# Optimization experiments

Measured on AMD Instinct MI355X. Metric: run time of the kernel, lower is better.

Reference implementation:

```python
import jax, jax.numpy as jnp
import numpy as np

B, T, D, H = 2, 2048, 1024, 16  # batch, seq, hidden, heads; head_dim = 64


def setup_inputs() -> dict:
    key = jax.random.key(0)
    k1, k2, k3 = jax.random.split(key, 3)
    X = jax.random.normal(k1, (B, T, D), dtype=jnp.float32)
    # Dense(3*hidden_dim, use_bias=False): kernel [D, 3D]
    Wqkv = jax.random.normal(k2, (D, 3 * D), dtype=jnp.float32) / np.float32(np.sqrt(D))
    # Dense(hidden_dim, use_bias=False): kernel [D, D]
    Wproj = jax.random.normal(k3, (D, D), dtype=jnp.float32) / np.float32(np.sqrt(D))
    return {"X": X, "Wqkv": Wqkv, "Wproj": Wproj, "train": 0}


def reference(X, Wqkv, Wproj, train):
    # train=0 -> dropout is identity; the chunked online-softmax in the
    # original is mathematically exact softmax causal attention.
    b, t, d = X.shape
    hd = d // H
    qkv = X @ Wqkv                      # [B,T,3D]
    q, k, v = jnp.split(qkv, 3, axis=-1)
    q = q.reshape(b, t, H, hd)
    k = k.reshape(b, t, H, hd)
    v = v.reshape(b, t, H, hd)
    scale = 1.0 / jnp.sqrt(jnp.asarray(hd, dtype=X.dtype))
    scores = jnp.einsum('bqhd,bkhd->bhqk', q * scale, k)  # [B,H,T,T]
    causal = jnp.tril(jnp.ones((t, t), dtype=bool))
    scores = jnp.where(causal[None, None, :, :], scores, -jnp.inf)
    attn = jax.nn.softmax(scores, axis=-1)
    out = jnp.einsum('bhqk,bkhd->bqhd', attn, v).reshape(b, t, d)
    return out @ Wproj
```

## Files before the change

### kernel.cpp

```cpp
#include <hip/hip_runtime.h>


using u16 = unsigned short;
using u32 = unsigned int;

typedef __bf16 bf16x8 __attribute__((ext_vector_type(8)));
typedef __bf16 bf16x2 __attribute__((ext_vector_type(2)));
typedef float f32x4 __attribute__((ext_vector_type(4)));

#define DEV __device__ __forceinline__

DEV u16 f2bf(float f) { __bf16 h = (__bf16)f; return *(u16*)&h; }

DEV float bf2f(u16 v) {
  union { u32 u; float f; } x; x.u = (u32)v << 16; return x.f;
}

DEV u32 pk2(float lo, float hi) {
  bf16x2 t = {(__bf16)lo, (__bf16)hi};
  return *(u32*)&t;
}

DEV f32x4 mfma16(bf16x8 a, bf16x8 b, f32x4 c) {
  return __builtin_amdgcn_mfma_f32_16x16x32_bf16(a, b, c, 0, 0, 0);
}

DEV void gload_lds16(const void* g, void* l) {
  __builtin_amdgcn_global_load_lds(
      (const __attribute__((address_space(1))) void*)g,
      (__attribute__((address_space(3))) void*)l, 16, 0, 0);
}

DEV bf16x8 ld16(const u16* p) { return *(const bf16x8*)p; }

DEV void BAR() {
  __builtin_amdgcn_s_barrier();
  __builtin_amdgcn_sched_barrier(0);
}

DEV int vperm(int slot) {
  return ((((slot >> 4) & 2) | ((slot >> 2) & 1)) << 4) + (((slot >> 3) & 3) << 2) + (slot & 3);
}
DEV int vperm_inv(int k) {
  return (k & 0x23) | ((k & 0x10) >> 2) | ((k & 0x0c) << 1);
}


__global__ __launch_bounds__(256) void prep_kernel(
    const float* __restrict__ X, u16* __restrict__ Xb,
    const float* __restrict__ Wqkv, u16* __restrict__ Wqkvt,
    const float* __restrict__ Wproj, u16* __restrict__ Wprojt) {
  const int bid = blockIdx.x;
  const int t = threadIdx.x;

  if (bid < 2048) {
    int i = (bid * 256 + t) * 8;
    float4 a = *(const float4*)&X[i];
    float4 b = *(const float4*)&X[i + 4];
    union { u16 u[8]; uint4 v; } o;
    o.u[0] = f2bf(a.x); o.u[1] = f2bf(a.y); o.u[2] = f2bf(a.z); o.u[3] = f2bf(a.w);
    o.u[4] = f2bf(b.x); o.u[5] = f2bf(b.y); o.u[6] = f2bf(b.z); o.u[7] = f2bf(b.w);
    *(uint4*)&Xb[i] = o.v;
    return;
  }

  __shared__ float tile[64][65];
  const float* W; u16* Wt; int C, tb;
  if (bid < 2816) { W = Wqkv;  Wt = Wqkvt;  C = 3072; tb = bid - 2048; }
  else            { W = Wproj; Wt = Wprojt; C = 1024; tb = bid - 2816; }
  const int tilesC = C >> 6;
  const int tr = tb / tilesC, tc = tb % tilesC;
#pragma unroll
  for (int j = 0; j < 16; ++j) {
    int idx = j * 256 + t;
    int r = idx >> 6, c = idx & 63;
    tile[r][c] = W[(tr * 64 + r) * C + tc * 64 + c];
  }
  __syncthreads();
#pragma unroll
  for (int j = 0; j < 16; ++j) {
    int idx = j * 256 + t;
    int r = idx >> 6, c = idx & 63;
    Wt[(tc * 64 + r) * 1024 + tr * 64 + c] = f2bf(tile[c][r]);
  }
}


__global__ __launch_bounds__(512, 2) void gemm256_qkv_kernel(
    const u16* __restrict__ A, const u16* __restrict__ Bt,
    u16* __restrict__ Qb, u16* __restrict__ Kb, u16* __restrict__ VtP) {
  int bid = blockIdx.x;
  int bid2 = (bid & 7) * 32 + (bid >> 3);
  const int mt = bid2 >> 4, nt = bid2 & 15;
  const int m0 = mt * 256, n0 = nt * 192;
  const int tid = threadIdx.x;
  const int wid = tid >> 6, lane = tid & 63;
  const int g = lane >> 4, li = lane & 15;
  const int wm = wid >> 2, wn = wid & 3;

  __shared__ __align__(16) u16 lds[57344];

  const int srow = lane >> 3;
  const int scol = ((lane & 7) * 8) ^ ((srow & 7) << 3);

  auto ISSUE_A = [&](int s, int kt) {
    const int p = kt & 1;
#pragma unroll
    for (int is2 = 0; is2 < 2; ++is2) {
      int row = is2 * 64 + wid * 8 + srow;
      gload_lds16(&A[(size_t)(m0 + s * 128 + row) * 1024 + kt * 64 + scol],
                  &lds[s * 16384 + p * 8192 + is2 * 4096 + wid * 512]);
    }
  };
  auto ISSUE_B = [&](int kt) {
    const int p = kt & 1;
#pragma unroll
    for (int j = 0; j < 3; ++j) {
      int chunk = wid * 3 + j;
      int row = chunk * 8 + srow;
      gload_lds16(&Bt[(size_t)(n0 + row) * 1024 + kt * 64 + scol],
                  &lds[32768 + p * 12288 + chunk * 512]);
    }
  };

  auto LDA = [&](int p, int ks, bf16x8* aF) {
#pragma unroll
    for (int mi = 0; mi < 8; ++mi) {
      int row = mi * 16 + li;
      aF[mi] = ld16(&lds[wm * 16384 + p * 8192 + row * 64 +
                         ((ks * 32 + g * 8) ^ ((li & 7) << 3))]);
    }
  };
  auto LDB = [&](int p, int ks, bf16x8* bF) {
#pragma unroll
    for (int ni = 0; ni < 3; ++ni) {
      int row = wn * 48 + ni * 16 + li;
      bF[ni] = ld16(&lds[32768 + p * 12288 + row * 64 +
                         ((ks * 32 + g * 8) ^ ((li & 7) << 3))]);
    }
  };

  f32x4 acc[8][3] = {};
  bf16x8 a0[8], a1[8], bF[3];

  ISSUE_A(0, 0); ISSUE_A(1, 0); ISSUE_B(0);
  ISSUE_A(0, 1); ISSUE_A(1, 1);
  asm volatile("s_waitcnt vmcnt(4)" ::: "memory");
  BAR();

  for (int t = 0; t < 16; ++t) {
    const int p = t & 1;
    LDB(p, 0, bF);
    LDA(p, 0, a0);
    if (t + 1 < 16) ISSUE_B(t + 1);
    BAR();
    __builtin_amdgcn_s_setprio(1);
#pragma unroll
    for (int mi = 0; mi < 4; ++mi)
#pragma unroll
      for (int ni = 0; ni < 3; ++ni)
        acc[mi][ni] = mfma16(a0[mi], bF[ni], acc[mi][ni]);
    __builtin_amdgcn_s_setprio(0);
    BAR();
    LDA(p, 1, a1);
    BAR();
    __builtin_amdgcn_s_setprio(1);
#pragma unroll
    for (int mi = 4; mi < 8; ++mi)
#pragma unroll
      for (int ni = 0; ni < 3; ++ni)
        acc[mi][ni] = mfma16(a0[mi], bF[ni], acc[mi][ni]);
    __builtin_amdgcn_s_setprio(0);
    BAR();
    LDB(p, 1, bF);
    BAR();
    __builtin_amdgcn_s_setprio(1);
#pragma unroll
    for (int mi = 0; mi < 4; ++mi)
#pragma unroll
      for (int ni = 0; ni < 3; ++ni)
        acc[mi][ni] = mfma16(a1[mi], bF[ni], acc[mi][ni]);
    __builtin_amdgcn_s_setprio(0);
    BAR();
    if (t + 2 < 16) { ISSUE_A(0, t + 2); ISSUE_A(1, t + 2); }
    BAR();
    __builtin_amdgcn_s_setprio(1);
#pragma unroll
    for (int mi = 4; mi < 8; ++mi)
#pragma unroll
      for (int ni = 0; ni < 3; ++ni)
        acc[mi][ni] = mfma16(a1[mi], bF[ni], acc[mi][ni]);
    __builtin_amdgcn_s_setprio(0);
    if (t + 2 < 16) {
      asm volatile("s_waitcnt vmcnt(4)" ::: "memory");
    } else {
      asm volatile("s_waitcnt vmcnt(0)" ::: "memory");
    }
    BAR();
  }

#pragma unroll
  for (int mi = 0; mi < 8; ++mi)
#pragma unroll
    for (int ni = 0; ni < 3; ++ni) {
      int cc = n0 + wn * 48 + ni * 16 + li;
      int which = cc >> 10, rem = cc & 1023;
      int h = rem >> 6, dd = rem & 63;
      int rbase = m0 + wm * 128 + mi * 16 + g * 4;
      int bb = rbase >> 11, tt = rbase & 2047;
      if (which == 2) {
        int slot0 = (tt & ~63) + vperm_inv(tt & 63);
        size_t di = ((size_t)(bb * 16 + h) * 64 + dd) * 2048 + slot0;
        uint2 wv;
        wv.x = pk2(acc[mi][ni][0], acc[mi][ni][1]);
        wv.y = pk2(acc[mi][ni][2], acc[mi][ni][3]);
        *(uint2*)&VtP[di] = wv;
      } else {
        u16* dst = which == 0 ? Qb : Kb;
        float sc = which == 0 ? 0.18033688f : 1.0f;
        size_t di = ((size_t)(bb * 16 + h) * 2048 + tt) * 64 + dd;
#pragma unroll
        for (int r = 0; r < 4; ++r) dst[di + (size_t)r * 64] = f2bf(acc[mi][ni][r] * sc);
      }
    }
}

__global__ __launch_bounds__(256) void gemm_proj_kernel(
    const u16* __restrict__ A, const u16* __restrict__ Bt, float* __restrict__ OF) {
  constexpr int NTN = 1024 / 128;
  const int mt = blockIdx.x / NTN, nt = blockIdx.x % NTN;
  const int m0 = mt * 128, n0 = nt * 128;
  const int tid = threadIdx.x;
  const int wid = tid >> 6, lane = tid & 63;
  const int g = lane >> 4, li = lane & 15;
  const int wm = wid >> 1, wn = wid & 1;

  __shared__ __align__(16) u16 As[2][128 * 64];
  __shared__ __align__(16) u16 Bs[2][128 * 64];

  f32x4 acc[4][4] = {};

  auto ISSUE = [&](int buf, int kt) {
#pragma unroll
    for (int iss = 0; iss < 4; ++iss) {
      int e = iss * 2048 + wid * 512 + lane * 8;
      int row = e >> 6;
      int kk = (e & 63) ^ ((row & 7) << 3);
      gload_lds16(&A[(size_t)(m0 + row) * 1024 + kt * 64 + kk], &As[buf][iss * 2048 + wid * 512]);
      gload_lds16(&Bt[(size_t)(n0 + row) * 1024 + kt * 64 + kk], &Bs[buf][iss * 2048 + wid * 512]);
    }
  };

  ISSUE(0, 0);
  __syncthreads();
  int cur = 0;

  for (int kt = 0; kt < 16; ++kt) {
    if (kt + 1 < 16) ISSUE(cur ^ 1, kt + 1);
#pragma unroll
    for (int ks = 0; ks < 2; ++ks) {
      bf16x8 af[4], bfr[4];
#pragma unroll
      for (int mi = 0; mi < 4; ++mi)
        af[mi] = ld16(&As[cur][(wm * 64 + mi * 16 + li) * 64 +
                               ((ks * 32 + g * 8) ^ ((li & 7) << 3))]);
#pragma unroll
      for (int ni = 0; ni < 4; ++ni)
        bfr[ni] = ld16(&Bs[cur][(wn * 64 + ni * 16 + li) * 64 +
                                ((ks * 32 + g * 8) ^ ((li & 7) << 3))]);
#pragma unroll
      for (int mi = 0; mi < 4; ++mi)
#pragma unroll
        for (int ni = 0; ni < 4; ++ni)
          acc[mi][ni] = mfma16(af[mi], bfr[ni], acc[mi][ni]);
    }
    __syncthreads();
    cur ^= 1;
  }

#pragma unroll
  for (int mi = 0; mi < 4; ++mi)
#pragma unroll
    for (int ni = 0; ni < 4; ++ni)
#pragma unroll
      for (int r = 0; r < 4; ++r) {
        int rr = m0 + wm * 64 + mi * 16 + g * 4 + r;
        int cc = n0 + wn * 64 + ni * 16 + li;
        OF[(size_t)rr * 1024 + cc] = acc[mi][ni][r];
      }
}


__global__ __launch_bounds__(256) void attn_kernel(const u16* __restrict__ Q,
                                                   const u16* __restrict__ K,
                                                   const u16* __restrict__ VtP,
                                                   u16* __restrict__ AO,
                                                   u16* __restrict__ P2O,
                                                   float* __restrict__ L1,
                                                   float* __restrict__ L2) {
  const int bid = blockIdx.x;
  const int idx = bid >> 5;
  const int qt = 31 - (idx >> 1);
  const int half = idx & 1;
  const int bh = bid & 31;
  const int b = bh >> 4, h = bh & 15;
  const int tid = threadIdx.x;
  const int wid = tid >> 6, lane = tid & 63;
  const int g = lane >> 4, li = lane & 15;
  const int q0 = qt * 64;
  const int kmid = (qt + 2) >> 1;
  const int k0 = half ? kmid : 0;
  const int k1 = half ? qt + 1 : kmid;

  if (k0 >= k1) {
    if (tid < 64) L2[(size_t)bh * 2048 + q0 + tid] = 0.f;
    return;
  }

  __shared__ __align__(16) u16 Ks[2][64 * 64];
  __shared__ __align__(16) u16 Vs[2][64 * 64];

  const u16* Qh = Q + (size_t)bh * 2048 * 64;
  const u16* Kh = K + (size_t)bh * 2048 * 64;
  const u16* Vh = VtP + (size_t)bh * 64 * 2048;

  const int qrow = q0 + wid * 16 + li;
  bf16x8 qf[2];
#pragma unroll
  for (int ks = 0; ks < 2; ++ks)
    qf[ks] = ld16(&Qh[(size_t)qrow * 64 + ks * 32 + g * 8]);

  f32x4 accO[4] = {};
  f32x4 accL = {};
  union { u32 u[4]; bf16x8 v; } ones;
  ones.u[0] = ones.u[1] = ones.u[2] = ones.u[3] = 0x3F803F80u;

  auto STAGE = [&](int buf, int ktile) {
#pragma unroll
    for (int iss = 0; iss < 2; ++iss) {
      int e = iss * 2048 + wid * 512 + lane * 8;
      int row = e >> 6;
      int c0 = (e & 63) ^ ((row & 7) << 3);
      gload_lds16(&Kh[(size_t)(ktile * 64 + row) * 64 + c0],
                  &Ks[buf][iss * 2048 + wid * 512]);
      gload_lds16(&Vh[(size_t)row * 2048 + ktile * 64 + c0],
                  &Vs[buf][iss * 2048 + wid * 512]);
    }
  };

  STAGE(0, k0);
  int cur = 0;

  for (int kt = k0; kt < k1; ++kt) {
    __syncthreads();
    if (kt + 1 < k1) STAGE(cur ^ 1, kt + 1);

    f32x4 s[4];
#pragma unroll
    for (int ni = 0; ni < 4; ++ni) s[ni] = f32x4{0.f, 0.f, 0.f, 0.f};
#pragma unroll
    for (int ks = 0; ks < 2; ++ks) {
      bf16x8 kf[4];
#pragma unroll
      for (int ni = 0; ni < 4; ++ni)
        kf[ni] = ld16(&Ks[cur][(ni * 16 + li) * 64 + ((ks * 32 + g * 8) ^ ((li & 7) << 3))]);
#pragma unroll
      for (int ni = 0; ni < 4; ++ni) s[ni] = mfma16(kf[ni], qf[ks], s[ni]);
    }

    if (kt == qt) {
      int ql = wid * 16 + li;
#pragma unroll
      for (int ni = 0; ni < 4; ++ni)
#pragma unroll
        for (int r = 0; r < 4; ++r)
          if (ni * 16 + g * 4 + r > ql) s[ni][r] = -1e30f;
    }

#pragma unroll
    for (int ni = 0; ni < 4; ++ni)
#pragma unroll
      for (int r = 0; r < 4; ++r) s[ni][r] = exp2f(s[ni][r]);

    union { u32 u[4]; bf16x8 v; } pf0, pf1;
    pf0.u[0] = pk2(s[0][0], s[0][1]); pf0.u[1] = pk2(s[0][2], s[0][3]);
    pf0.u[2] = pk2(s[1][0], s[1][1]); pf0.u[3] = pk2(s[1][2], s[1][3]);
    pf1.u[0] = pk2(s[2][0], s[2][1]); pf1.u[1] = pk2(s[2][2], s[2][3]);
    pf1.u[2] = pk2(s[3][0], s[3][1]); pf1.u[3] = pk2(s[3][2], s[3][3]);

    accL = mfma16(ones.v, pf0.v, accL);
    accL = mfma16(ones.v, pf1.v, accL);

#pragma unroll
    for (int ks = 0; ks < 2; ++ks) {
      bf16x8 pf = ks ? pf1.v : pf0.v;
#pragma unroll
      for (int mi = 0; mi < 4; ++mi) {
        bf16x8 vf = ld16(&Vs[cur][(mi * 16 + li) * 64 + ((ks * 32 + g * 8) ^ ((li & 7) << 3))]);
        accO[mi] = mfma16(vf, pf, accO[mi]);
      }
    }
    cur ^= 1;
  }

  if (g == 0) (half ? L2 : L1)[(size_t)bh * 2048 + qrow] = accL[0];
  __syncthreads();
  u16* E = (u16*)Ks;
  int erow = wid * 16 + li;
#pragma unroll
  for (int mi = 0; mi < 4; ++mi) {
    uint2 wv;
    wv.x = pk2(accO[mi][0], accO[mi][1]);
    wv.y = pk2(accO[mi][2], accO[mi][3]);
    *(uint2*)&E[erow * 64 + ((mi * 16 + g * 4) ^ ((li & 7) << 3))] = wv;
  }
  __syncthreads();
#pragma unroll
  for (int pass = 0; pass < 2; ++pass) {
    int idx2 = pass * 2048 + tid * 8;
    int row = idx2 >> 6, col = idx2 & 63;
    uint4 val = *(uint4*)&E[row * 64 + (col ^ ((row & 7) << 3))];
    if (half == 0)
      *(uint4*)&AO[(size_t)(b * 2048 + q0 + row) * 1024 + h * 64 + col] = val;
    else
      *(uint4*)&P2O[((size_t)bh * 2048 + q0 + row) * 64 + col] = val;
  }
}

__global__ __launch_bounds__(256) void combine_kernel(u16* __restrict__ AO,
                                                      const u16* __restrict__ P2O,
                                                      const float* __restrict__ L1,
                                                      const float* __restrict__ L2) {
  int gid = blockIdx.x * 256 + threadIdx.x;
  int row = gid >> 3, dp = (gid & 7) * 8;
  int bh = row >> 11, q = row & 2047;
  int b = bh >> 4, h = bh & 15;
  float l2 = L2[row];
  float inv = 1.0f / (L1[row] + l2);
  float w2 = (l2 == 0.f) ? 0.f : inv;
  u16* ao = &AO[(size_t)(b * 2048 + q) * 1024 + h * 64 + dp];
  const u16* p2 = &P2O[(size_t)row * 64 + dp];
  union { uint4 v; u16 u[8]; } o1, o2, w;
  o1.v = *(const uint4*)ao;
  o2.v = *(const uint4*)p2;
#pragma unroll
  for (int j = 0; j < 8; ++j)
    w.u[j] = f2bf(bf2f(o1.u[j]) * inv + bf2f(o2.u[j]) * w2);
  *(uint4*)ao = w.v;
}


extern "C" void kernel_launch(void* const* d_in, const int* in_sizes, int n_in,
                              void* d_out, int out_size, void* d_ws, size_t ws_size,
                              hipStream_t stream) {
  const float* X = (const float*)d_in[0];
  const float* Wqkv = (const float*)d_in[1];
  const float* Wproj = (const float*)d_in[2];
  float* out = (float*)d_out;

  u16* ws = (u16*)d_ws;
  u16* Xb = ws;
  u16* Wqkvt = Xb + 4194304;
  u16* Wprojt = Wqkvt + 3145728;
  u16* Qb = Wprojt + 1048576;
  u16* Kb = Qb + 4194304;
  u16* VtP = Kb + 4194304;
  u16* AO = VtP + 4194304;
  u16* P2O = Xb;
  float* L1 = (float*)Wqkvt;
  float* L2 = L1 + 65536;

  prep_kernel<<<3072, 256, 0, stream>>>(X, Xb, Wqkv, Wqkvt, Wproj, Wprojt);
  gemm256_qkv_kernel<<<256, 512, 0, stream>>>(Xb, Wqkvt, Qb, Kb, VtP);
  attn_kernel<<<2048, 256, 0, stream>>>(Qb, Kb, VtP, AO, P2O, L1, L2);
  combine_kernel<<<2048, 256, 0, stream>>>(AO, P2O, L1, L2);
  gemm_proj_kernel<<<32 * 8, 256, 0, stream>>>(AO, Wprojt, out);
}
```

Baseline: 104.5 us.

## Process 128 query rows per attention block to reuse K/V fragments

Each attention block now covers 128 query rows instead of 64. Each wave handles two 16-row query groups that share the K and V fragments read from LDS, which halves LDS traffic and staging per query row. The key-range split between the two halves is redefined so each half gets exactly qt+1 tiles, which removes the empty-block path, and the grid is halved. In exchange, per-thread register use roughly doubles (accumulators and preloaded K/V fragments), which may lower occupancy, and fewer blocks run in total.

```diff
diff --git a/kernel.cpp b/kernel.cpp
--- a/kernel.cpp
+++ b/kernel.cpp
@@ -299,23 +299,16 @@
                                                    float* __restrict__ L1,
                                                    float* __restrict__ L2) {
   const int bid = blockIdx.x;
-  const int idx = bid >> 5;
-  const int qt = 31 - (idx >> 1);
-  const int half = idx & 1;
+  const int qt = 15 - (bid >> 6);
+  const int half = (bid >> 5) & 1;
   const int bh = bid & 31;
   const int b = bh >> 4, h = bh & 15;
   const int tid = threadIdx.x;
   const int wid = tid >> 6, lane = tid & 63;
   const int g = lane >> 4, li = lane & 15;
-  const int q0 = qt * 64;
-  const int kmid = (qt + 2) >> 1;
-  const int k0 = half ? kmid : 0;
-  const int k1 = half ? qt + 1 : kmid;
-
-  if (k0 >= k1) {
-    if (tid < 64) L2[(size_t)bh * 2048 + q0 + tid] = 0.f;
-    return;
-  }
+  const int q0 = qt * 128;
+  const int k0 = half ? qt + 1 : 0;
+  const int k1 = half ? 2 * qt + 2 : qt + 1;
 
   __shared__ __align__(16) u16 Ks[2][64 * 64];
   __shared__ __align__(16) u16 Vs[2][64 * 64];
@@ -324,14 +317,17 @@
   const u16* Kh = K + (size_t)bh * 2048 * 64;
   const u16* Vh = VtP + (size_t)bh * 64 * 2048;
 
-  const int qrow = q0 + wid * 16 + li;
-  bf16x8 qf[2];
-#pragma unroll
-  for (int ks = 0; ks < 2; ++ks)
-    qf[ks] = ld16(&Qh[(size_t)qrow * 64 + ks * 32 + g * 8]);
-
-  f32x4 accO[4] = {};
-  f32x4 accL = {};
+  const int qa = q0 + wid * 32 + li;
+  const int qb = qa + 16;
+  bf16x8 qfa[2], qfb[2];
+#pragma unroll
+  for (int ks = 0; ks < 2; ++ks) {
+    qfa[ks] = ld16(&Qh[(size_t)qa * 64 + ks * 32 + g * 8]);
+    qfb[ks] = ld16(&Qh[(size_t)qb * 64 + ks * 32 + g * 8]);
+  }
+
+  f32x4 accA[4] = {}, accB[4] = {};
+  f32x4 accLA = {}, accLB = {};
   union { u32 u[4]; bf16x8 v; } ones;
   ones.u[0] = ones.u[1] = ones.u[2] = ones.u[3] = 0x3F803F80u;
 
@@ -355,68 +351,94 @@
     __syncthreads();
     if (kt + 1 < k1) STAGE(cur ^ 1, kt + 1);
 
-    f32x4 s[4];
-#pragma unroll
-    for (int ni = 0; ni < 4; ++ni) s[ni] = f32x4{0.f, 0.f, 0.f, 0.f};
-#pragma unroll
-    for (int ks = 0; ks < 2; ++ks) {
-      bf16x8 kf[4];
+    bf16x8 kf[8], vf[8];
+#pragma unroll
+    for (int ni = 0; ni < 4; ++ni) {
+      kf[ni]     = ld16(&Ks[cur][(ni * 16 + li) * 64 + ((g * 8) ^ ((li & 7) << 3))]);
+      kf[4 + ni] = ld16(&Ks[cur][(ni * 16 + li) * 64 + ((32 + g * 8) ^ ((li & 7) << 3))]);
+    }
+#pragma unroll
+    for (int mi = 0; mi < 4; ++mi) {
+      vf[mi]     = ld16(&Vs[cur][(mi * 16 + li) * 64 + ((g * 8) ^ ((li & 7) << 3))]);
+      vf[4 + mi] = ld16(&Vs[cur][(mi * 16 + li) * 64 + ((32 + g * 8) ^ ((li & 7) << 3))]);
+    }
+
+    f32x4 sA[4], sB[4];
+#pragma unroll
+    for (int ni = 0; ni < 4; ++ni) { sA[ni] = f32x4{0,0,0,0}; sB[ni] = f32x4{0,0,0,0}; }
+#pragma unroll
+    for (int ni = 0; ni < 4; ++ni) {
+      sA[ni] = mfma16(kf[ni], qfa[0], sA[ni]);
+      sA[ni] = mfma16(kf[4 + ni], qfa[1], sA[ni]);
+      sB[ni] = mfma16(kf[ni], qfb[0], sB[ni]);
+      sB[ni] = mfma16(kf[4 + ni], qfb[1], sB[ni]);
+    }
+
+    if (kt >= 2 * qt) {
 #pragma unroll
       for (int ni = 0; ni < 4; ++ni)
-        kf[ni] = ld16(&Ks[cur][(ni * 16 + li) * 64 + ((ks * 32 + g * 8) ^ ((li & 7) << 3))]);
-#pragma unroll
-      for (int ni = 0; ni < 4; ++ni) s[ni] = mfma16(kf[ni], qf[ks], s[ni]);
-    }
-
-    if (kt == qt) {
-      int ql = wid * 16 + li;
-#pragma unroll
-      for (int ni = 0; ni < 4; ++ni)
-#pragma unroll
-        for (int r = 0; r < 4; ++r)
-          if (ni * 16 + g * 4 + r > ql) s[ni][r] = -1e30f;
+#pragma unroll
+        for (int r = 0; r < 4; ++r) {
+          int kg = kt * 64 + ni * 16 + g * 4 + r;
+          if (kg > qa) sA[ni][r] = -1e30f;
+          if (kg > qb) sB[ni][r] = -1e30f;
+        }
     }
 
 #pragma unroll
     for (int ni = 0; ni < 4; ++ni)
 #pragma unroll
-      for (int r = 0; r < 4; ++r) s[ni][r] = exp2f(s[ni][r]);
-
-    union { u32 u[4]; bf16x8 v; } pf0, pf1;
-    pf0.u[0] = pk2(s[0][0], s[0][1]); pf0.u[1] = pk2(s[0][2], s[0][3]);
-    pf0.u[2] = pk2(s[1][0], s[1][1]); pf0.u[3] = pk2(s[1][2], s[1][3]);
-    pf1.u[0] = pk2(s[2][0], s[2][1]); pf1.u[1] = pk2(s[2][2], s[2][3]);
-    pf1.u[2] = pk2(s[3][0], s[3][1]); pf1.u[3] = pk2(s[3][2], s[3][3]);
-
-    accL = mfma16(ones.v, pf0.v, accL);
-    accL = mfma16(ones.v, pf1.v, accL);
-
-#pragma unroll
-    for (int ks = 0; ks < 2; ++ks) {
-      bf16x8 pf = ks ? pf1.v : pf0.v;
-#pragma unroll
-      for (int mi = 0; mi < 4; ++mi) {
-        bf16x8 vf = ld16(&Vs[cur][(mi * 16 + li) * 64 + ((ks * 32 + g * 8) ^ ((li & 7) << 3))]);
-        accO[mi] = mfma16(vf, pf, accO[mi]);
+      for (int r = 0; r < 4; ++r) {
+        sA[ni][r] = exp2f(sA[ni][r]);
+        sB[ni][r] = exp2f(sB[ni][r]);
       }
+
+    union { u32 u[4]; bf16x8 v; } pA0, pA1, pB0, pB1;
+    pA0.u[0] = pk2(sA[0][0], sA[0][1]); pA0.u[1] = pk2(sA[0][2], sA[0][3]);
+    pA0.u[2] = pk2(sA[1][0], sA[1][1]); pA0.u[3] = pk2(sA[1][2], sA[1][3]);
+    pA1.u[0] = pk2(sA[2][0], sA[2][1]); pA1.u[1] = pk2(sA[2][2], sA[2][3]);
+    pA1.u[2] = pk2(sA[3][0], sA[3][1]); pA1.u[3] = pk2(sA[3][2], sA[3][3]);
+    pB0.u[0] = pk2(sB[0][0], sB[0][1]); pB0.u[1] = pk2(sB[0][2], sB[0][3]);
+    pB0.u[2] = pk2(sB[1][0], sB[1][1]); pB0.u[3] = pk2(sB[1][2], sB[1][3]);
+    pB1.u[0] = pk2(sB[2][0], sB[2][1]); pB1.u[1] = pk2(sB[2][2], sB[2][3]);
+    pB1.u[2] = pk2(sB[3][0], sB[3][1]); pB1.u[3] = pk2(sB[3][2], sB[3][3]);
+
+    accLA = mfma16(ones.v, pA0.v, accLA);
+    accLA = mfma16(ones.v, pA1.v, accLA);
+    accLB = mfma16(ones.v, pB0.v, accLB);
+    accLB = mfma16(ones.v, pB1.v, accLB);
+
+#pragma unroll
+    for (int mi = 0; mi < 4; ++mi) {
+      accA[mi] = mfma16(vf[mi], pA0.v, accA[mi]);
+      accA[mi] = mfma16(vf[4 + mi], pA1.v, accA[mi]);
+      accB[mi] = mfma16(vf[mi], pB0.v, accB[mi]);
+      accB[mi] = mfma16(vf[4 + mi], pB1.v, accB[mi]);
     }
     cur ^= 1;
   }
 
-  if (g == 0) (half ? L2 : L1)[(size_t)bh * 2048 + qrow] = accL[0];
+  if (g == 0) {
+    float* L = half ? L2 : L1;
+    L[(size_t)bh * 2048 + qa] = accLA[0];
+    L[(size_t)bh * 2048 + qb] = accLB[0];
+  }
   __syncthreads();
   u16* E = (u16*)Ks;
-  int erow = wid * 16 + li;
+  int ea = wid * 32 + li, eb = ea + 16;
 #pragma unroll
   for (int mi = 0; mi < 4; ++mi) {
-    uint2 wv;
-    wv.x = pk2(accO[mi][0], accO[mi][1]);
-    wv.y = pk2(accO[mi][2], accO[mi][3]);
-    *(uint2*)&E[erow * 64 + ((mi * 16 + g * 4) ^ ((li & 7) << 3))] = wv;
+    uint2 wa, wb;
+    wa.x = pk2(accA[mi][0], accA[mi][1]);
+    wa.y = pk2(accA[mi][2], accA[mi][3]);
+    wb.x = pk2(accB[mi][0], accB[mi][1]);
+    wb.y = pk2(accB[mi][2], accB[mi][3]);
+    *(uint2*)&E[ea * 64 + ((mi * 16 + g * 4) ^ ((li & 7) << 3))] = wa;
+    *(uint2*)&E[eb * 64 + ((mi * 16 + g * 4) ^ ((li & 7) << 3))] = wb;
   }
   __syncthreads();
 #pragma unroll
-  for (int pass = 0; pass < 2; ++pass) {
+  for (int pass = 0; pass < 4; ++pass) {
     int idx2 = pass * 2048 + tid * 8;
     int row = idx2 >> 6, col = idx2 & 63;
     uint4 val = *(uint4*)&E[row * 64 + (col ^ ((row & 7) << 3))];
@@ -472,7 +494,7 @@
 
   prep_kernel<<<3072, 256, 0, stream>>>(X, Xb, Wqkv, Wqkvt, Wproj, Wprojt);
   gemm256_qkv_kernel<<<256, 512, 0, stream>>>(Xb, Wqkvt, Qb, Kb, VtP);
-  attn_kernel<<<2048, 256, 0, stream>>>(Qb, Kb, VtP, AO, P2O, L1, L2);
+  attn_kernel<<<1024, 256, 0, stream>>>(Qb, Kb, VtP, AO, P2O, L1, L2);
   combine_kernel<<<2048, 256, 0, stream>>>(AO, P2O, L1, L2);
   gemm_proj_kernel<<<32 * 8, 256, 0, stream>>>(AO, Wprojt, out);
 }
```

Result: slower. 109.2 us (+4.5%).
